# Performance work log

Measured on AMD Instinct MI355X. Metric: run time of the kernel, lower is better.

Reference implementation:

```python
import jax, jax.numpy as jnp
import numpy as np

B, DIM, H = 65536, 1024, 16
HD = DIM // H  # head dim = 64


def setup_inputs() -> dict:
    key = jax.random.key(0)
    ks = jax.random.split(key, 6)
    x = jax.random.normal(ks[0], (B, DIM), dtype=jnp.float32)
    y = jax.random.normal(ks[1], (B, DIM), dtype=jnp.float32)
    mask = jnp.zeros((B,), dtype=jnp.bool_)  # unused by the module
    # Parameters (qkv_bias=False -> no bias on q/kv; proj has bias)
    Wq = jax.random.normal(ks[2], (DIM, DIM), dtype=jnp.float32) * 0.02
    Wkv = jax.random.normal(ks[3], (DIM, 2 * DIM), dtype=jnp.float32) * 0.02
    Wproj = jax.random.normal(ks[4], (DIM, DIM), dtype=jnp.float32) * 0.02
    bproj = jax.random.normal(ks[5], (DIM,), dtype=jnp.float32) * 0.02
    return {"x": x, "y": y, "mask": mask, "Wq": Wq, "Wkv": Wkv,
            "Wproj": Wproj, "bproj": bproj}


def reference(x, y, mask, Wq, Wkv, Wproj, bproj):
    # mask is accepted but unused, matching the original module.
    scale = HD ** (-0.5)
    q = x @ Wq                      # [B, DIM]
    kv = y @ Wkv                    # [B, 2*DIM]
    k, v = jnp.split(kv, 2, axis=-1)
    # b (h d) -> b h d
    q = q.reshape(B, H, HD) * scale  # first scale (q *= scale)
    k = k.reshape(B, H, HD)
    v = v.reshape(B, H, HD)
    # per-head dot product, scaled AGAIN (faithful to original double-scale)
    dots = jnp.einsum("bhd,bhd->bh", q, k) * scale  # [B, H]
    attn = jax.nn.softmax(dots, axis=-1)             # softmax over heads
    out = attn[..., None] * v                        # [B, H, HD]
    out = out.reshape(B, DIM)                        # b h d -> b (h d)
    return out @ Wproj + bproj
```

## Files before the change

kernel.cpp:

```cpp
#include <hip/hip_runtime.h>

typedef unsigned short ushort_t;
typedef unsigned int   uint_t;

typedef ushort_t u16x8  __attribute__((ext_vector_type(8)));
typedef __bf16   bf16x8 __attribute__((ext_vector_type(8)));
typedef float    f32x4  __attribute__((ext_vector_type(4)));

#define DIMSZ 1024
#define NT 16

__device__ __forceinline__ ushort_t f2bf(float f) {
  uint_t u = __builtin_bit_cast(uint_t, f);
  u += 0x7fffu + ((u >> 16) & 1u);
  return (ushort_t)(u >> 16);
}
__device__ __forceinline__ float bf2f(ushort_t h) {
  uint_t u = ((uint_t)h) << 16;
  return __builtin_bit_cast(float, u);
}
__device__ __forceinline__ void lds_load16(const void* g, void* l) {
  __builtin_amdgcn_global_load_lds((const __attribute__((address_space(1))) void*)g,
                                   (__attribute__((address_space(3))) void*)l, 16, 0, 0);
}
#define SCHED0() __builtin_amdgcn_sched_barrier(0)
#define WBAR() do { SCHED0(); __builtin_amdgcn_s_barrier(); SCHED0(); } while (0)

__global__ __launch_bounds__(256) void wtrans(const float* __restrict__ src, int ld,
                                              ushort_t* __restrict__ dst) {
  __shared__ ushort_t tile[32][33];
  const int bx = blockIdx.x;
  const int by = blockIdx.y;
  const int tx = threadIdx.x & 31, ty = threadIdx.x >> 5;
#pragma unroll
  for (int i = 0; i < 32; i += 8)
    tile[ty + i][tx] = f2bf(src[(size_t)(by * 32 + ty + i) * ld + bx * 32 + tx]);
  __syncthreads();
#pragma unroll
  for (int i = 0; i < 32; i += 8)
    dst[(size_t)(bx * 32 + ty + i) * 1024 + by * 32 + tx] = tile[tx][ty + i];
}

__global__ __launch_bounds__(256) void cvt_bf16(const float* __restrict__ s,
                                                ushort_t* __restrict__ d) {
  const size_t n8 = (size_t)65536 * 1024 / 8;
  const size_t stride = (size_t)gridDim.x * 256;
  for (size_t i = (size_t)blockIdx.x * 256 + threadIdx.x; i < n8; i += stride) {
    f32x4 f0 = *(const f32x4*)(s + i * 8);
    f32x4 f1 = *(const f32x4*)(s + i * 8 + 4);
    u16x8 o;
#pragma unroll
    for (int j = 0; j < 4; ++j) { o[j] = f2bf(f0[j]); o[4 + j] = f2bf(f1[j]); }
    *(u16x8*)(d + i * 8) = o;
  }
}

__global__ __launch_bounds__(256) void attn_k(ushort_t* __restrict__ qb,
                                              const ushort_t* __restrict__ kvb) {
  const int idx = blockIdx.x * 256 + threadIdx.x;
  const int row = idx >> 4, h = idx & 15;
  const ushort_t* qp = qb + (size_t)row * 1024 + h * 64;
  const ushort_t* kp = kvb + (size_t)row * 2048 + h * 64;
  const ushort_t* vp = kp + 1024;
  float s = 0.f;
#pragma unroll
  for (int i = 0; i < 64; i += 8) {
    u16x8 q8 = *(const u16x8*)(qp + i);
    u16x8 k8 = *(const u16x8*)(kp + i);
#pragma unroll
    for (int j = 0; j < 8; ++j) s += bf2f(q8[j]) * bf2f(k8[j]);
  }
  s *= 0.015625f;
  float m = s;
#pragma unroll
  for (int off = 8; off >= 1; off >>= 1) m = fmaxf(m, __shfl_xor(m, off, 16));
  float e = expf(s - m);
  float sum = e;
#pragma unroll
  for (int off = 8; off >= 1; off >>= 1) sum += __shfl_xor(sum, off, 16);
  const float wgt = e / sum;
  ushort_t* op = qb + (size_t)row * 1024 + h * 64;
#pragma unroll
  for (int i = 0; i < 64; i += 8) {
    u16x8 v8 = *(const u16x8*)(vp + i);
    u16x8 o8;
#pragma unroll
    for (int j = 0; j < 8; ++j) o8[j] = f2bf(bf2f(v8[j]) * wgt);
    *(u16x8*)(op + i) = o8;
  }
}

template <int OUTF32>
__global__ __launch_bounds__(512, 2) void gemm8(const ushort_t* __restrict__ A,
                                                const ushort_t* __restrict__ Bt,
                                                void* __restrict__ Cv,
                                                const float* __restrict__ bias,
                                                int ldc, int ncol_lg2) {
  __shared__ ushort_t lds[65536];
  const int t = threadIdx.x;
  const int nb8 = gridDim.x >> 3;
  const int nbid = (blockIdx.x & 7) * nb8 + (blockIdx.x >> 3);
  const int n0 = (nbid & ((1 << ncol_lg2) - 1)) * 256;
  const int m0 = (nbid >> ncol_lg2) * 256;
  const int w = t >> 6, lane = t & 63;
  const int wm = w >> 2, wn = w & 3;
  const int lr = lane & 15, lk = lane >> 4;
  const int w512 = w * 512;

  const int srow = w * 8 + (lane >> 3);
  const int scsw = ((lane & 7) * 16) ^ ((srow & 7) << 4);
  const ushort_t* aS = A + (size_t)(m0 + srow) * DIMSZ + (scsw >> 1);
  const ushort_t* bS = Bt + (size_t)(n0 + srow) * DIMSZ + (scsw >> 1);

  const int cbe0 = (((lk * 16)) ^ ((lr & 7) << 4)) >> 1;
  const int cbe1 = ((64 + lk * 16) ^ ((lr & 7) << 4)) >> 1;
  const int aRB = lr * 64;
  const int bRB = 32768 + (wn * 64 + lr) * 64;

  f32x4 acc[8][4];
  const f32x4 zf = {0.f, 0.f, 0.f, 0.f};
#pragma unroll
  for (int i = 0; i < 8; ++i)
#pragma unroll
    for (int j = 0; j < 4; ++j) acc[i][j] = zf;
  bf16x8 a[4][2], b0[2][2], b1[2][2];

#define STAGE_A(cc, hh, tt) do {                                          \
    const ushort_t* s_ = aS + (size_t)(hh) * 65536 + (tt) * 64;           \
    ushort_t* d_ = lds + (cc) * 16384 + (hh) * 4096 + w512;               \
    lds_load16(s_, d_);                                                   \
    lds_load16(s_ + 131072, d_ + 8192); } while (0)
#define STAGE_B(cc, hh, tt) do {                                          \
    const ushort_t* s_ = bS + (size_t)(hh) * 131072 + (tt) * 64;          \
    ushort_t* d_ = lds + 32768 + (cc) * 16384 + (hh) * 8192 + w512;       \
    lds_load16(s_, d_);                                                   \
    lds_load16(s_ + 65536, d_ + 4096); } while (0)
#define LDA(cc, mq) do {                                                  \
    const ushort_t* Lp = lds + (cc) * 16384 + (wm * 2 + (mq)) * 4096 + aRB; \
    _Pragma("unroll") for (int j = 0; j < 4; ++j) {                       \
      a[j][0] = *(const bf16x8*)(Lp + j * 1024 + cbe0);                   \
      a[j][1] = *(const bf16x8*)(Lp + j * 1024 + cbe1); } } while (0)
#define LDB(cc, dst, nq) do {                                             \
    const ushort_t* Lp = lds + (cc) * 16384 + bRB + (nq) * 2048;          \
    _Pragma("unroll") for (int ni = 0; ni < 2; ++ni) {                    \
      dst[ni][0] = *(const bf16x8*)(Lp + ni * 1024 + cbe0);               \
      dst[ni][1] = *(const bf16x8*)(Lp + ni * 1024 + cbe1); } } while (0)
#define MMQ(mb, B, nb) do {                                               \
    _Pragma("unroll") for (int j = 0; j < 4; ++j)                         \
    _Pragma("unroll") for (int ni = 0; ni < 2; ++ni)                      \
    _Pragma("unroll") for (int ks = 0; ks < 2; ++ks)                      \
      acc[(mb) + j][(nb) + ni] = __builtin_amdgcn_mfma_f32_16x16x32_bf16( \
          a[j][ks], B[ni][ks], acc[(mb) + j][(nb) + ni], 0, 0, 0); } while (0)
#define TILE(S1, S2, VM, tv, c, nxt) do {                                 \
    LDA(c, 0); LDB(c, b0, 0);                                             \
    if (S1) STAGE_A(nxt, 1, (tv) + 1);                                    \
    WBAR();                                                               \
    __builtin_amdgcn_s_setprio(1); MMQ(0, b0, 0); __builtin_amdgcn_s_setprio(0); \
    WBAR();                                                               \
    LDB(c, b1, 1);                                                        \
    if (S2) STAGE_A(c, 0, (tv) + 2);                                      \
    WBAR();                                                               \
    __builtin_amdgcn_s_setprio(1); MMQ(0, b1, 2); __builtin_amdgcn_s_setprio(0); \
    WBAR();                                                               \
    LDA(c, 1);                                                            \
    if (S2) STAGE_B(c, 0, (tv) + 2);                                      \
    WBAR();                                                               \
    __builtin_amdgcn_s_setprio(1); MMQ(4, b1, 2); __builtin_amdgcn_s_setprio(0); \
    WBAR();                                                               \
    if (S2) STAGE_B(c, 1, (tv) + 2);                                      \
    if ((VM) == 6) { asm volatile("s_waitcnt vmcnt(6)" ::: "memory"); }   \
    else if ((VM) == 0) { asm volatile("s_waitcnt vmcnt(0)" ::: "memory"); } \
    WBAR();                                                               \
    __builtin_amdgcn_s_setprio(1); MMQ(4, b0, 0); __builtin_amdgcn_s_setprio(0); \
    WBAR();                                                               \
  } while (0)

  STAGE_A(0, 0, 0); STAGE_A(0, 1, 0); STAGE_B(0, 0, 0); STAGE_B(0, 1, 0);
  STAGE_A(1, 0, 1); STAGE_B(1, 0, 1); STAGE_B(1, 1, 1);
  asm volatile("s_waitcnt vmcnt(6)" ::: "memory");
  WBAR();

  for (int tt = 0; tt < 7; ++tt) {
    const int t0 = tt * 2;
    TILE(1, 1, 6, t0, 0, 1);
    TILE(1, 1, 6, t0 + 1, 1, 0);
  }
  TILE(1, 0, 0, 14, 0, 1);
  TILE(0, 0, -1, 15, 1, 0);

#undef TILE
#undef MMQ
#undef LDB
#undef LDA
#undef STAGE_B
#undef STAGE_A

  if (!OUTF32) {
    ushort_t* Cp = (ushort_t*)Cv;
    ushort_t* ep = lds + w * 8192;
#pragma unroll
    for (int mq = 0; mq < 2; ++mq)
#pragma unroll
      for (int j = 0; j < 4; ++j)
#pragma unroll
        for (int ni = 0; ni < 4; ++ni)
#pragma unroll
          for (int r = 0; r < 4; ++r) {
            const int row = mq * 64 + j * 16 + lk * 4 + r;
            const int ce = ((ni * 16 + lr) * 2) ^ ((row & 7) << 4);
            ep[row * 64 + (ce >> 1)] = f2bf(acc[mq * 4 + j][ni][r]);
          }
#pragma unroll
    for (int rr = 0; rr < 16; ++rr) {
      const int row = rr * 8 + (lane >> 3);
      const int ce = ((lane & 7) * 16) ^ ((lane >> 3) << 4);
      u16x8 vv = *(const u16x8*)(ep + row * 64 + (ce >> 1));
      *(u16x8*)(Cp + (size_t)(m0 + wm * 128 + row) * ldc + n0 + wn * 64 + (lane & 7) * 8) = vv;
    }
  } else {
    float* Op = (float*)Cv;
    float bb[4];
#pragma unroll
    for (int ni = 0; ni < 4; ++ni) bb[ni] = bias[n0 + wn * 64 + ni * 16 + lr];
#pragma unroll
    for (int mq = 0; mq < 2; ++mq)
#pragma unroll
      for (int j = 0; j < 4; ++j)
#pragma unroll
        for (int ni = 0; ni < 4; ++ni)
#pragma unroll
          for (int r = 0; r < 4; ++r)
            Op[(size_t)(m0 + wm * 128 + mq * 64 + j * 16 + lk * 4 + r) * 1024 +
               n0 + wn * 64 + ni * 16 + lr] = acc[mq * 4 + j][ni][r] + bb[ni];
  }
}

extern "C" void kernel_launch(void* const* d_in, const int* in_sizes, int n_in,
                              void* d_out, int out_size, void* d_ws, size_t ws_size,
                              hipStream_t stream) {
  const float* x   = (const float*)d_in[0];
  const float* y   = (const float*)d_in[1];
  const float* Wq  = (const float*)d_in[3];
  const float* Wkv = (const float*)d_in[4];
  const float* Wp  = (const float*)d_in[5];
  const float* bp  = (const float*)d_in[6];
  (void)in_sizes; (void)n_in; (void)out_size; (void)ws_size;

  char* ws = (char*)d_ws;
  ushort_t* Wqt  = (ushort_t*)(ws);
  ushort_t* Wkvt = (ushort_t*)(ws + (2ull   << 20));
  ushort_t* Wpt  = (ushort_t*)(ws + (6ull   << 20));
  ushort_t* qb   = (ushort_t*)(ws + (8ull   << 20));
  ushort_t* kvb  = (ushort_t*)(ws + (136ull << 20));
  ushort_t* actb = (ushort_t*)(ws + (392ull << 20));

  wtrans<<<dim3(32, 32), 256, 0, stream>>>(Wq, 1024, Wqt);
  wtrans<<<dim3(64, 32), 256, 0, stream>>>(Wkv, 2048, Wkvt);
  wtrans<<<dim3(32, 32), 256, 0, stream>>>(Wp, 1024, Wpt);

  cvt_bf16<<<4096, 256, 0, stream>>>(y, actb);
  gemm8<0><<<2048, 512, 0, stream>>>(actb, Wkvt, kvb, nullptr, 2048, 3);

  cvt_bf16<<<4096, 256, 0, stream>>>(x, actb);
  gemm8<0><<<1024, 512, 0, stream>>>(actb, Wqt, qb, nullptr, 1024, 2);

  attn_k<<<4096, 256, 0, stream>>>(qb, kvb);

  gemm8<1><<<1024, 512, 0, stream>>>(qb, Wpt, d_out, bp, 1024, 2);
}
```

Before: 915.7 us.

## Fuse fp32-to-bf16 conversion and attention-weighting into GEMM A-operand loading

Removes the separate cvt_bf16 passes by having the GEMM load fp32 activations into registers and convert them to bf16 while writing LDS. The attention kernel now writes only per-head softmax weights. The output projection GEMM reads V straight from the kv buffer and scales it by those weights during A staging. This cuts several full-size activation round trips through HBM. In exchange, A-operand staging switches from async global-to-LDS loads to register loads with manual conversion, which adds VGPR pressure, VALU work and different wait scheduling inside the pipelined loop.

```diff
diff --git a/kernel.cpp b/kernel.cpp
--- a/kernel.cpp
+++ b/kernel.cpp
@@ -3,12 +3,13 @@
 typedef unsigned short ushort_t;
 typedef unsigned int   uint_t;
 
+typedef ushort_t u16x4  __attribute__((ext_vector_type(4)));
 typedef ushort_t u16x8  __attribute__((ext_vector_type(8)));
+typedef __bf16   bf16x4 __attribute__((ext_vector_type(4)));
 typedef __bf16   bf16x8 __attribute__((ext_vector_type(8)));
 typedef float    f32x4  __attribute__((ext_vector_type(4)));
 
 #define DIMSZ 1024
-#define NT 16
 
 __device__ __forceinline__ ushort_t f2bf(float f) {
   uint_t u = __builtin_bit_cast(uint_t, f);
@@ -29,8 +30,7 @@
 __global__ __launch_bounds__(256) void wtrans(const float* __restrict__ src, int ld,
                                               ushort_t* __restrict__ dst) {
   __shared__ ushort_t tile[32][33];
-  const int bx = blockIdx.x;
-  const int by = blockIdx.y;
+  const int bx = blockIdx.x, by = blockIdx.y;
   const int tx = threadIdx.x & 31, ty = threadIdx.x >> 5;
 #pragma unroll
   for (int i = 0; i < 32; i += 8)
@@ -41,27 +41,13 @@
     dst[(size_t)(bx * 32 + ty + i) * 1024 + by * 32 + tx] = tile[tx][ty + i];
 }
 
-__global__ __launch_bounds__(256) void cvt_bf16(const float* __restrict__ s,
-                                                ushort_t* __restrict__ d) {
-  const size_t n8 = (size_t)65536 * 1024 / 8;
-  const size_t stride = (size_t)gridDim.x * 256;
-  for (size_t i = (size_t)blockIdx.x * 256 + threadIdx.x; i < n8; i += stride) {
-    f32x4 f0 = *(const f32x4*)(s + i * 8);
-    f32x4 f1 = *(const f32x4*)(s + i * 8 + 4);
-    u16x8 o;
-#pragma unroll
-    for (int j = 0; j < 4; ++j) { o[j] = f2bf(f0[j]); o[4 + j] = f2bf(f1[j]); }
-    *(u16x8*)(d + i * 8) = o;
-  }
-}
-
-__global__ __launch_bounds__(256) void attn_k(ushort_t* __restrict__ qb,
-                                              const ushort_t* __restrict__ kvb) {
+__global__ __launch_bounds__(256) void attn_lite(const ushort_t* __restrict__ qb,
+                                                 const ushort_t* __restrict__ kvb,
+                                                 float* __restrict__ attn) {
   const int idx = blockIdx.x * 256 + threadIdx.x;
   const int row = idx >> 4, h = idx & 15;
   const ushort_t* qp = qb + (size_t)row * 1024 + h * 64;
   const ushort_t* kp = kvb + (size_t)row * 2048 + h * 64;
-  const ushort_t* vp = kp + 1024;
   float s = 0.f;
 #pragma unroll
   for (int i = 0; i < 64; i += 8) {
@@ -78,24 +64,16 @@
   float sum = e;
 #pragma unroll
   for (int off = 8; off >= 1; off >>= 1) sum += __shfl_xor(sum, off, 16);
-  const float wgt = e / sum;
-  ushort_t* op = qb + (size_t)row * 1024 + h * 64;
-#pragma unroll
-  for (int i = 0; i < 64; i += 8) {
-    u16x8 v8 = *(const u16x8*)(vp + i);
-    u16x8 o8;
-#pragma unroll
-    for (int j = 0; j < 8; ++j) o8[j] = f2bf(bf2f(v8[j]) * wgt);
-    *(u16x8*)(op + i) = o8;
-  }
-}
-
-template <int OUTF32>
-__global__ __launch_bounds__(512, 2) void gemm8(const ushort_t* __restrict__ A,
+  attn[idx] = e / sum;
+}
+
+template <int AMODE, int OUTF32>
+__global__ __launch_bounds__(512, 2) void gemm8(const void* __restrict__ Aq,
+                                                const float* __restrict__ attnp,
                                                 const ushort_t* __restrict__ Bt,
                                                 void* __restrict__ Cv,
                                                 const float* __restrict__ bias,
-                                                int ldc, int ncol_lg2) {
+                                                int lda, int ldc, int ncol_lg2) {
   __shared__ ushort_t lds[65536];
   const int t = threadIdx.x;
   const int nb8 = gridDim.x >> 3;
@@ -109,10 +87,15 @@
 
   const int srow = w * 8 + (lane >> 3);
   const int scsw = ((lane & 7) * 16) ^ ((srow & 7) << 4);
-  const ushort_t* aS = A + (size_t)(m0 + srow) * DIMSZ + (scsw >> 1);
   const ushort_t* bS = Bt + (size_t)(n0 + srow) * DIMSZ + (scsw >> 1);
 
-  const int cbe0 = (((lk * 16)) ^ ((lr & 7) << 4)) >> 1;
+  const int sr_base = w * 32 + lk;
+  const int sc4 = lr * 4;
+  const float*    aF  = (const float*)Aq + (size_t)(m0 + sr_base) * lda + sc4;
+  const ushort_t* aH  = (const ushort_t*)Aq + (size_t)(m0 + sr_base) * lda + sc4;
+  const float*    atS = attnp ? (attnp + (size_t)(m0 + sr_base) * 16) : (const float*)Aq;
+
+  const int cbe0 = ((lk * 16) ^ ((lr & 7) << 4)) >> 1;
   const int cbe1 = ((64 + lk * 16) ^ ((lr & 7) << 4)) >> 1;
   const int aRB = lr * 64;
   const int bRB = 32768 + (wn * 64 + lr) * 64;
@@ -124,17 +107,35 @@
 #pragma unroll
     for (int j = 0; j < 4; ++j) acc[i][j] = zf;
   bf16x8 a[4][2], b0[2][2], b1[2][2];
-
-#define STAGE_A(cc, hh, tt) do {                                          \
-    const ushort_t* s_ = aS + (size_t)(hh) * 65536 + (tt) * 64;           \
-    ushort_t* d_ = lds + (cc) * 16384 + (hh) * 4096 + w512;               \
-    lds_load16(s_, d_);                                                   \
-    lds_load16(s_ + 131072, d_ + 8192); } while (0)
+  f32x4 areg[8];
+  u16x4 vreg[8];
+  float sreg[8];
+
+#define LOADA(tt) do {                                                    \
+    if constexpr (AMODE == 0) {                                           \
+      _Pragma("unroll") for (int s = 0; s < 8; ++s)                       \
+        areg[s] = *(const f32x4*)(aF + (size_t)s * 4 * lda + (tt) * 64);  \
+    } else {                                                              \
+      _Pragma("unroll") for (int s = 0; s < 8; ++s) {                     \
+        vreg[s] = *(const u16x4*)(aH + (size_t)s * 4 * lda + (tt) * 64);  \
+        sreg[s] = atS[s * 64 + (tt)]; } } } while (0)
+#define CVTW(bc) do {                                                     \
+    _Pragma("unroll") for (int s = 0; s < 8; ++s) {                       \
+      const int r_ = sr_base + s * 4;                                     \
+      char* dp_ = (char*)lds + (size_t)((bc) * 32768 + r_ * 128 +         \
+                  ((sc4 * 2) ^ ((r_ & 7) << 4)));                         \
+      bf16x4 o_;                                                          \
+      if constexpr (AMODE == 0) {                                         \
+        _Pragma("unroll") for (int j = 0; j < 4; ++j) o_[j] = (__bf16)areg[s][j]; \
+      } else {                                                            \
+        _Pragma("unroll") for (int j = 0; j < 4; ++j)                     \
+          o_[j] = (__bf16)(bf2f(vreg[s][j]) * sreg[s]); }                 \
+      *(bf16x4*)dp_ = o_; } } while (0)
 #define STAGE_B(cc, hh, tt) do {                                          \
-    const ushort_t* s_ = bS + (size_t)(hh) * 131072 + (tt) * 64;          \
+    const ushort_t* s_ = bS + (size_t)(hh) * (128 * DIMSZ) + (tt) * 64;   \
     ushort_t* d_ = lds + 32768 + (cc) * 16384 + (hh) * 8192 + w512;       \
     lds_load16(s_, d_);                                                   \
-    lds_load16(s_ + 65536, d_ + 4096); } while (0)
+    lds_load16(s_ + 64 * DIMSZ, d_ + 4096); } while (0)
 #define LDA(cc, mq) do {                                                  \
     const ushort_t* Lp = lds + (cc) * 16384 + (wm * 2 + (mq)) * 4096 + aRB; \
     _Pragma("unroll") for (int j = 0; j < 4; ++j) {                       \
@@ -151,49 +152,59 @@
     _Pragma("unroll") for (int ks = 0; ks < 2; ++ks)                      \
       acc[(mb) + j][(nb) + ni] = __builtin_amdgcn_mfma_f32_16x16x32_bf16( \
           a[j][ks], B[ni][ks], acc[(mb) + j][(nb) + ni], 0, 0, 0); } while (0)
-#define TILE(S1, S2, VM, tv, c, nxt) do {                                 \
+#define TILE(IA, SB, VM, CV, tv, c) do {                                  \
     LDA(c, 0); LDB(c, b0, 0);                                             \
-    if (S1) STAGE_A(nxt, 1, (tv) + 1);                                    \
+    if (IA) LOADA((tv) + 1);                                              \
     WBAR();                                                               \
     __builtin_amdgcn_s_setprio(1); MMQ(0, b0, 0); __builtin_amdgcn_s_setprio(0); \
     WBAR();                                                               \
     LDB(c, b1, 1);                                                        \
-    if (S2) STAGE_A(c, 0, (tv) + 2);                                      \
     WBAR();                                                               \
     __builtin_amdgcn_s_setprio(1); MMQ(0, b1, 2); __builtin_amdgcn_s_setprio(0); \
     WBAR();                                                               \
     LDA(c, 1);                                                            \
-    if (S2) STAGE_B(c, 0, (tv) + 2);                                      \
+    if (SB) STAGE_B(c, 0, (tv) + 2);                                      \
     WBAR();                                                               \
     __builtin_amdgcn_s_setprio(1); MMQ(4, b1, 2); __builtin_amdgcn_s_setprio(0); \
     WBAR();                                                               \
-    if (S2) STAGE_B(c, 1, (tv) + 2);                                      \
-    if ((VM) == 6) { asm volatile("s_waitcnt vmcnt(6)" ::: "memory"); }   \
-    else if ((VM) == 0) { asm volatile("s_waitcnt vmcnt(0)" ::: "memory"); } \
+    if (SB) STAGE_B(c, 1, (tv) + 2);                                      \
+    if ((VM) == 4)      asm volatile("s_waitcnt vmcnt(4)" ::: "memory");  \
+    else if ((VM) == 0) asm volatile("s_waitcnt vmcnt(0)" ::: "memory");  \
+    if (CV) { CVTW((c) ^ 1);                                              \
+      asm volatile("s_waitcnt lgkmcnt(0)" ::: "memory"); }                \
     WBAR();                                                               \
     __builtin_amdgcn_s_setprio(1); MMQ(4, b0, 0); __builtin_amdgcn_s_setprio(0); \
     WBAR();                                                               \
   } while (0)
 
-  STAGE_A(0, 0, 0); STAGE_A(0, 1, 0); STAGE_B(0, 0, 0); STAGE_B(0, 1, 0);
-  STAGE_A(1, 0, 1); STAGE_B(1, 0, 1); STAGE_B(1, 1, 1);
-  asm volatile("s_waitcnt vmcnt(6)" ::: "memory");
+  LOADA(0);
+  STAGE_B(0, 0, 0); STAGE_B(0, 1, 0);
+  asm volatile("s_waitcnt vmcnt(4)" ::: "memory");
+  CVTW(0);
+  LOADA(1);
+  STAGE_B(1, 0, 1); STAGE_B(1, 1, 1);
+  if constexpr (AMODE == 0) asm volatile("s_waitcnt vmcnt(12)" ::: "memory");
+  else                      asm volatile("s_waitcnt vmcnt(20)" ::: "memory");
+  asm volatile("s_waitcnt lgkmcnt(0)" ::: "memory");
   WBAR();
 
-  for (int tt = 0; tt < 7; ++tt) {
-    const int t0 = tt * 2;
-    TILE(1, 1, 6, t0, 0, 1);
-    TILE(1, 1, 6, t0 + 1, 1, 0);
+  TILE(0, 1, 4, 1, 0, 0);
+  for (int tt2 = 0; tt2 < 6; ++tt2) {
+    const int tv = tt2 * 2 + 1;
+    TILE(1, 1, 4, 1, tv, 1);
+    TILE(1, 1, 4, 1, tv + 1, 0);
   }
-  TILE(1, 0, 0, 14, 0, 1);
-  TILE(0, 0, -1, 15, 1, 0);
+  TILE(1, 1, 4, 1, 13, 1);
+  TILE(1, 0, 0, 1, 14, 0);
+  TILE(0, 0, -1, 0, 15, 1);
 
 #undef TILE
 #undef MMQ
 #undef LDB
 #undef LDA
 #undef STAGE_B
-#undef STAGE_A
+#undef CVTW
+#undef LOADA
 
   if (!OUTF32) {
     ushort_t* Cp = (ushort_t*)Cv;
@@ -247,24 +258,22 @@
   (void)in_sizes; (void)n_in; (void)out_size; (void)ws_size;
 
   char* ws = (char*)d_ws;
-  ushort_t* Wqt  = (ushort_t*)(ws);
-  ushort_t* Wkvt = (ushort_t*)(ws + (2ull   << 20));
-  ushort_t* Wpt  = (ushort_t*)(ws + (6ull   << 20));
-  ushort_t* qb   = (ushort_t*)(ws + (8ull   << 20));
-  ushort_t* kvb  = (ushort_t*)(ws + (136ull << 20));
-  ushort_t* actb = (ushort_t*)(ws + (392ull << 20));
+  ushort_t* Wqt   = (ushort_t*)(ws);
+  ushort_t* Wkvt  = (ushort_t*)(ws + (2ull   << 20));
+  ushort_t* Wpt   = (ushort_t*)(ws + (6ull   << 20));
+  float*    attnb = (float*)   (ws + (8ull   << 20));
+  ushort_t* qb    = (ushort_t*)(ws + (12ull  << 20));
+  ushort_t* kvb   = (ushort_t*)(ws + (140ull << 20));
 
   wtrans<<<dim3(32, 32), 256, 0, stream>>>(Wq, 1024, Wqt);
   wtrans<<<dim3(64, 32), 256, 0, stream>>>(Wkv, 2048, Wkvt);
   wtrans<<<dim3(32, 32), 256, 0, stream>>>(Wp, 1024, Wpt);
 
-  cvt_bf16<<<4096, 256, 0, stream>>>(y, actb);
-  gemm8<0><<<2048, 512, 0, stream>>>(actb, Wkvt, kvb, nullptr, 2048, 3);
-
-  cvt_bf16<<<4096, 256, 0, stream>>>(x, actb);
-  gemm8<0><<<1024, 512, 0, stream>>>(actb, Wqt, qb, nullptr, 1024, 2);
-
-  attn_k<<<4096, 256, 0, stream>>>(qb, kvb);
-
-  gemm8<1><<<1024, 512, 0, stream>>>(qb, Wpt, d_out, bp, 1024, 2);
-}
+  gemm8<0, 0><<<2048, 512, 0, stream>>>((const void*)y, nullptr, Wkvt, kvb, nullptr,
+                                        1024, 2048, 3);
+  gemm8<0, 0><<<1024, 512, 0, stream>>>((const void*)x, nullptr, Wqt, qb, nullptr,
+                                        1024, 1024, 2);
+  attn_lite<<<4096, 256, 0, stream>>>(qb, kvb, attnb);
+  gemm8<1, 1><<<1024, 512, 0, stream>>>((const void*)(kvb + 1024), attnb, Wpt, d_out, bp,
+                                        2048, 1024, 2);
+}
```

After: 1.072 ms. 17.0% more time.

## Fuse q·k per-head dot into Q GEMM epilogue, drop Q materialization

Applied to the files above, without the earlier changes.

The Q projection GEMM no longer writes Q to memory. Its epilogue loads the matching K slice into LDS and computes the per-head dot products directly from the fp32 accumulators, writing only a [B,16] dots buffer. A small softmax kernel normalizes the dots, and a separate kernel scales V by the weights into the bf16 activation buffer for the output projection. This removes the 128MB Q write and read and the old attention kernel's Q traffic, at the cost of an extra K read in the epilogue and one more small launch.

```diff
diff --git a/kernel.cpp b/kernel.cpp
--- a/kernel.cpp
+++ b/kernel.cpp
@@ -8,7 +8,6 @@
 typedef float    f32x4  __attribute__((ext_vector_type(4)));
 
 #define DIMSZ 1024
-#define NT 16
 
 __device__ __forceinline__ ushort_t f2bf(float f) {
   uint_t u = __builtin_bit_cast(uint_t, f);
@@ -29,8 +28,7 @@
 __global__ __launch_bounds__(256) void wtrans(const float* __restrict__ src, int ld,
                                               ushort_t* __restrict__ dst) {
   __shared__ ushort_t tile[32][33];
-  const int bx = blockIdx.x;
-  const int by = blockIdx.y;
+  const int bx = blockIdx.x, by = blockIdx.y;
   const int tx = threadIdx.x & 31, ty = threadIdx.x >> 5;
 #pragma unroll
   for (int i = 0; i < 32; i += 8)
@@ -55,46 +53,52 @@
   }
 }
 
-__global__ __launch_bounds__(256) void attn_k(ushort_t* __restrict__ qb,
-                                              const ushort_t* __restrict__ kvb) {
-  const int idx = blockIdx.x * 256 + threadIdx.x;
-  const int row = idx >> 4, h = idx & 15;
-  const ushort_t* qp = qb + (size_t)row * 1024 + h * 64;
-  const ushort_t* kp = kvb + (size_t)row * 2048 + h * 64;
-  const ushort_t* vp = kp + 1024;
-  float s = 0.f;
-#pragma unroll
-  for (int i = 0; i < 64; i += 8) {
-    u16x8 q8 = *(const u16x8*)(qp + i);
-    u16x8 k8 = *(const u16x8*)(kp + i);
-#pragma unroll
-    for (int j = 0; j < 8; ++j) s += bf2f(q8[j]) * bf2f(k8[j]);
-  }
-  s *= 0.015625f;
-  float m = s;
-#pragma unroll
-  for (int off = 8; off >= 1; off >>= 1) m = fmaxf(m, __shfl_xor(m, off, 16));
-  float e = expf(s - m);
-  float sum = e;
-#pragma unroll
-  for (int off = 8; off >= 1; off >>= 1) sum += __shfl_xor(sum, off, 16);
-  const float wgt = e / sum;
-  ushort_t* op = qb + (size_t)row * 1024 + h * 64;
-#pragma unroll
-  for (int i = 0; i < 64; i += 8) {
-    u16x8 v8 = *(const u16x8*)(vp + i);
-    u16x8 o8;
-#pragma unroll
-    for (int j = 0; j < 8; ++j) o8[j] = f2bf(bf2f(v8[j]) * wgt);
-    *(u16x8*)(op + i) = o8;
-  }
-}
-
-template <int OUTF32>
+__global__ __launch_bounds__(256) void softmax16(float* __restrict__ d) {
+  const int row = blockIdx.x * 256 + threadIdx.x;
+  f32x4 v[4];
+#pragma unroll
+  for (int i = 0; i < 4; ++i) v[i] = *(const f32x4*)(d + (size_t)row * 16 + i * 4);
+  float m = v[0][0];
+#pragma unroll
+  for (int i = 0; i < 4; ++i)
+#pragma unroll
+    for (int j = 0; j < 4; ++j) m = fmaxf(m, v[i][j]);
+  float sum = 0.f;
+#pragma unroll
+  for (int i = 0; i < 4; ++i)
+#pragma unroll
+    for (int j = 0; j < 4; ++j) { v[i][j] = expf(v[i][j] - m); sum += v[i][j]; }
+  const float r = 1.f / sum;
+#pragma unroll
+  for (int i = 0; i < 4; ++i) {
+#pragma unroll
+    for (int j = 0; j < 4; ++j) v[i][j] *= r;
+    *(f32x4*)(d + (size_t)row * 16 + i * 4) = v[i];
+  }
+}
+
+__global__ __launch_bounds__(256) void abk(const ushort_t* __restrict__ kvb,
+                                           const float* __restrict__ at,
+                                           ushort_t* __restrict__ ab) {
+  const size_t stride = (size_t)gridDim.x * 256;
+  for (size_t g = (size_t)blockIdx.x * 256 + threadIdx.x; g < (size_t)8388608; g += stride) {
+    const int row = (int)(g >> 7), c8 = (int)(g & 127);
+    const float sc = at[(size_t)row * 16 + (c8 >> 3)];
+    u16x8 v8 = *(const u16x8*)(kvb + (size_t)row * 2048 + 1024 + c8 * 8);
+    u16x8 o;
+#pragma unroll
+    for (int j = 0; j < 8; ++j) o[j] = f2bf(bf2f(v8[j]) * sc);
+    *(u16x8*)(ab + (size_t)row * 1024 + c8 * 8) = o;
+  }
+}
+
+template <int EPI>
 __global__ __launch_bounds__(512, 2) void gemm8(const ushort_t* __restrict__ A,
                                                 const ushort_t* __restrict__ Bt,
                                                 void* __restrict__ Cv,
                                                 const float* __restrict__ bias,
+                                                const ushort_t* __restrict__ kvp,
+                                                float* __restrict__ dots,
                                                 int ldc, int ncol_lg2) {
   __shared__ ushort_t lds[65536];
   const int t = threadIdx.x;
@@ -195,7 +199,7 @@
 #undef STAGE_B
 #undef STAGE_A
 
-  if (!OUTF32) {
+  if constexpr (EPI == 0) {
     ushort_t* Cp = (ushort_t*)Cv;
     ushort_t* ep = lds + w * 8192;
 #pragma unroll
@@ -217,7 +221,7 @@
       u16x8 vv = *(const u16x8*)(ep + row * 64 + (ce >> 1));
       *(u16x8*)(Cp + (size_t)(m0 + wm * 128 + row) * ldc + n0 + wn * 64 + (lane & 7) * 8) = vv;
     }
-  } else {
+  } else if constexpr (EPI == 1) {
     float* Op = (float*)Cv;
     float bb[4];
 #pragma unroll
@@ -232,6 +236,31 @@
           for (int r = 0; r < 4; ++r)
             Op[(size_t)(m0 + wm * 128 + mq * 64 + j * 16 + lk * 4 + r) * 1024 +
                n0 + wn * 64 + ni * 16 + lr] = acc[mq * 4 + j][ni][r] + bb[ni];
+  } else {
+    const int h = (n0 >> 6) + wn;
+    ushort_t* kw = lds + w * 8192;
+    const int rsub = lane >> 3, c8 = (lane & 7) * 8;
+    const ushort_t* kS = kvp + (size_t)(m0 + wm * 128 + rsub) * 2048 + h * 64 + c8;
+#pragma unroll
+    for (int i = 0; i < 16; ++i)
+      lds_load16(kS + (size_t)i * 8 * 2048, kw + i * 512);
+    asm volatile("s_waitcnt vmcnt(0)" ::: "memory");
+#pragma unroll
+    for (int mq = 0; mq < 2; ++mq)
+#pragma unroll
+      for (int j = 0; j < 4; ++j)
+#pragma unroll
+        for (int r = 0; r < 4; ++r) {
+          const int row = mq * 64 + j * 16 + lk * 4 + r;
+          float p = 0.f;
+#pragma unroll
+          for (int ni = 0; ni < 4; ++ni)
+            p += acc[mq * 4 + j][ni][r] * bf2f(kw[row * 64 + ni * 16 + lr]);
+#pragma unroll
+          for (int off = 1; off < 16; off <<= 1) p += __shfl_xor(p, off, 16);
+          if (lr == 0)
+            dots[(size_t)(m0 + wm * 128 + row) * 16 + h] = p * 0.015625f;
+        }
   }
 }
 
@@ -247,24 +276,26 @@
   (void)in_sizes; (void)n_in; (void)out_size; (void)ws_size;
 
   char* ws = (char*)d_ws;
-  ushort_t* Wqt  = (ushort_t*)(ws);
-  ushort_t* Wkvt = (ushort_t*)(ws + (2ull   << 20));
-  ushort_t* Wpt  = (ushort_t*)(ws + (6ull   << 20));
-  ushort_t* qb   = (ushort_t*)(ws + (8ull   << 20));
-  ushort_t* kvb  = (ushort_t*)(ws + (136ull << 20));
-  ushort_t* actb = (ushort_t*)(ws + (392ull << 20));
+  ushort_t* Wqt   = (ushort_t*)(ws);
+  ushort_t* Wkvt  = (ushort_t*)(ws + (2ull   << 20));
+  ushort_t* Wpt   = (ushort_t*)(ws + (6ull   << 20));
+  float*    dotsb = (float*)   (ws + (8ull   << 20));
+  ushort_t* kvb   = (ushort_t*)(ws + (12ull  << 20));
+  ushort_t* actb  = (ushort_t*)(ws + (268ull << 20));
 
   wtrans<<<dim3(32, 32), 256, 0, stream>>>(Wq, 1024, Wqt);
   wtrans<<<dim3(64, 32), 256, 0, stream>>>(Wkv, 2048, Wkvt);
   wtrans<<<dim3(32, 32), 256, 0, stream>>>(Wp, 1024, Wpt);
 
   cvt_bf16<<<4096, 256, 0, stream>>>(y, actb);
-  gemm8<0><<<2048, 512, 0, stream>>>(actb, Wkvt, kvb, nullptr, 2048, 3);
+  gemm8<0><<<2048, 512, 0, stream>>>(actb, Wkvt, kvb, nullptr, nullptr, nullptr, 2048, 3);
 
   cvt_bf16<<<4096, 256, 0, stream>>>(x, actb);
-  gemm8<0><<<1024, 512, 0, stream>>>(actb, Wqt, qb, nullptr, 1024, 2);
-
-  attn_k<<<4096, 256, 0, stream>>>(qb, kvb);
-
-  gemm8<1><<<1024, 512, 0, stream>>>(qb, Wpt, d_out, bp, 1024, 2);
-}
+  gemm8<2><<<1024, 512, 0, stream>>>(actb, Wqt, nullptr, nullptr, kvb, dotsb, 1024, 2);
+
+  softmax16<<<256, 256, 0, stream>>>(dotsb);
+
+  abk<<<2048, 256, 0, stream>>>(kvb, dotsb, actb);
+
+  gemm8<1><<<1024, 512, 0, stream>>>(actb, Wpt, d_out, bp, nullptr, nullptr, 1024, 2);
+}
```

New measurement: 813.6 us. -11.1%, faster.
